# Optimization experiments

Hardware: AMD Instinct MI355X
Metric: run time of the kernel (lower is better)

## Reference

```python
import jax, jax.numpy as jnp
import numpy as np

N = 100000
CIN = 32
COUT = 64
K = 16          # n_kernels (height bins)
STRIDE = 1
DIM = 1         # height coordinate column
XG, ZG, BG = 256, 256, 4   # BEV grid extents and batch size


def setup_inputs() -> dict:
    key = jax.random.key(0)
    k0, k1, k2, k3, k4, k5 = jax.random.split(key, 6)
    feats = jax.random.normal(k0, (N, CIN), dtype=jnp.float32)
    x = jax.random.randint(k1, (N,), 0, XG)
    y = jax.random.randint(k2, (N,), 0, K * STRIDE)
    z = jax.random.randint(k3, (N,), 0, ZG)
    b = jax.random.randint(k4, (N,), 0, BG)
    coords = jnp.stack([x, y, z, b], axis=1).astype(jnp.int32)  # [N,4]
    std = 1.0 / np.sqrt(CIN)
    kernel = jax.random.uniform(k5, (K, CIN, COUT), dtype=jnp.float32,
                                minval=-std, maxval=std)
    return {"feats": feats, "coords": coords, "kernel": kernel}


def reference(feats, coords, kernel):
    # Per-point kernel selection by (quantized) height coordinate.
    idx = coords[:, DIM].astype(jnp.int32) // STRIDE          # [N]
    per_point = kernel[idx]                                   # [N,Cin,Cout] gather
    out = jnp.einsum('ni,nio->no', feats, per_point)          # [N,Cout]
    # Coalesce: zero the height coord and scatter-add duplicate BEV coords.
    # (stride==1 so no spatial re-quantization branch.)
    lin = (coords[:, 3].astype(jnp.int32) * XG + coords[:, 0]) * ZG + coords[:, 2]
    bev = jax.ops.segment_sum(out, lin, num_segments=BG * XG * ZG)  # [B*X*Z,Cout]
    return bev
```

## Files before the change

### kernel.cpp

```cpp
#include <hip/hip_runtime.h>

#define CIN   32
#define COUT  64
#define XG    256
#define ZG    256

__global__ __launch_bounds__(256) void tobev_kernel(
    const float* __restrict__ feats,
    const int*   __restrict__ coords,
    const float* __restrict__ kern,
    float* __restrict__ out,
    int n)
{
    const int wid  = blockIdx.x * 4 + (threadIdx.x >> 6);
    const int lane = threadIdx.x & 63;
    if (wid >= n) return;

    const int4 c = *reinterpret_cast<const int4*>(coords + wid * 4);
    const int idx = c.y;
    const int lin = (c.w * XG + c.x) * ZG + c.z;

    const float f = feats[wid * CIN + (lane & 31)];
    const float* __restrict__ w = kern + idx * (CIN * COUT) + lane;

    float acc = 0.f;
    #pragma unroll
    for (int i = 0; i < CIN; ++i) {
        const float fi = __shfl(f, i, 64);
        acc = fmaf(fi, w[(size_t)i * COUT], acc);
    }

    unsafeAtomicAdd(&out[(size_t)lin * COUT + lane], acc);
}

extern "C" void kernel_launch(void* const* d_in, const int* in_sizes, int n_in,
                              void* d_out, int out_size, void* d_ws, size_t ws_size,
                              hipStream_t stream) {
    const float* feats  = (const float*)d_in[0];
    const int*   coords = (const int*)d_in[1];
    const float* kern   = (const float*)d_in[2];
    float* out = (float*)d_out;

    const int n = in_sizes[0] / CIN;

    hipMemsetAsync(d_out, 0, (size_t)out_size * sizeof(float), stream);

    const int blocks = (n + 3) / 4;
    hipLaunchKernelGGL(tobev_kernel, dim3(blocks), dim3(256), 0, stream,
                       feats, coords, kern, out, n);
}
```

Before: 52.67 us.

## Bucket points by height kernel per wave, keeping weights in registers

Each wave is now assigned one of the K height bins plus a chunk of 256 points. It loads that bin's 32x64 weight slice into registers once, scans the chunk's coords and ballots the points that match, then processes only those. This replaces a per-point gather of the 8KB weight slice with register reuse. The cost is that coords are read K times over, there are K times as many waves, and the serial ballot loop adds control overhead.

```diff
diff --git a/kernel.cpp b/kernel.cpp
--- a/kernel.cpp
+++ b/kernel.cpp
@@ -4,33 +4,51 @@
 #define COUT  64
 #define XG    256
 #define ZG    256
+#define K     16
+#define CHUNK 256
 
-__global__ __launch_bounds__(256) void tobev_kernel(
+__global__ __launch_bounds__(256, 6) void tobev_kernel(
     const float* __restrict__ feats,
     const int*   __restrict__ coords,
     const float* __restrict__ kern,
     float* __restrict__ out,
-    int n)
+    int n, int nchunks)
 {
-    const int wid  = blockIdx.x * 4 + (threadIdx.x >> 6);
+    const int g    = blockIdx.x * 4 + (threadIdx.x >> 6);
     const int lane = threadIdx.x & 63;
-    if (wid >= n) return;
+    const int b    = g / nchunks;
+    const int chunk = g - b * nchunks;
+    if (b >= K) return;
 
-    const int4 c = *reinterpret_cast<const int4*>(coords + wid * 4);
-    const int idx = c.y;
-    const int lin = (c.w * XG + c.x) * ZG + c.z;
+    float w[CIN];
+    #pragma unroll
+    for (int i = 0; i < CIN; ++i)
+        w[i] = kern[(size_t)b * (CIN * COUT) + i * COUT + lane];
 
-    const float f = feats[wid * CIN + (lane & 31)];
-    const float* __restrict__ w = kern + idx * (CIN * COUT) + lane;
+    const int base = chunk * CHUNK;
 
-    float acc = 0.f;
-    #pragma unroll
-    for (int i = 0; i < CIN; ++i) {
-        const float fi = __shfl(f, i, 64);
-        acc = fmaf(fi, w[(size_t)i * COUT], acc);
+    for (int j = 0; j < CHUNK / 64; ++j) {
+        const int p = base + j * 64 + lane;
+        int idx = -1, lin = 0;
+        if (p < n) {
+            const int4 c = *reinterpret_cast<const int4*>(coords + (size_t)p * 4);
+            idx = c.y;
+            lin = (c.w * XG + c.x) * ZG + c.z;
+        }
+        unsigned long long mask = __ballot(idx == b);
+        while (mask) {
+            const int s = __ffsll(mask) - 1;
+            mask &= mask - 1;
+            const int   ps   = base + j * 64 + s;
+            const int   lins = __shfl(lin, s, 64);
+            const float f    = feats[(size_t)ps * CIN + (lane & 31)];
+            float acc = 0.f;
+            #pragma unroll
+            for (int i = 0; i < CIN; ++i)
+                acc = fmaf(__shfl(f, i, 64), w[i], acc);
+            unsafeAtomicAdd(&out[(size_t)lins * COUT + lane], acc);
+        }
     }
-
-    unsafeAtomicAdd(&out[(size_t)lin * COUT + lane], acc);
 }
 
 extern "C" void kernel_launch(void* const* d_in, const int* in_sizes, int n_in,
@@ -45,7 +63,9 @@
 
     hipMemsetAsync(d_out, 0, (size_t)out_size * sizeof(float), stream);
 
-    const int blocks = (n + 3) / 4;
+    const int nchunks = (n + CHUNK - 1) / CHUNK;
+    const int nwaves  = K * nchunks;
+    const int blocks  = (nwaves + 3) / 4;
     hipLaunchKernelGGL(tobev_kernel, dim3(blocks), dim3(256), 0, stream,
-                       feats, coords, kern, out, n);
+                       feats, coords, kern, out, n, nchunks);
 }
```

Result: slower. 76.89 us (+46.0%).

## Bucket points per BEV cell and compute segment sums without output atomics

Applied to the files above, without the earlier changes.

Replaces the per-point atomic scatter with a three-phase scheme. First, points are binned into fixed-capacity slots per BEV cell using counters, with an overflow list for crowded cells. Second, one wave per cell accumulates its points and writes the output directly, with half of the kernel weights staged in LDS. Third, a single block atomically adds the overflow points. This removes the output memset and atomics, but adds a workspace pass, a full-grid sweep over all cells (mostly empty), a single-block serial overflow kernel, and a silent cap on overflow entries.

```diff
diff --git a/kernel.cpp b/kernel.cpp
--- a/kernel.cpp
+++ b/kernel.cpp
@@ -1,11 +1,100 @@
 #include <hip/hip_runtime.h>
 
-#define CIN   32
-#define COUT  64
-#define XG    256
-#define ZG    256
+#define CIN    32
+#define COUT   64
+#define XG     256
+#define ZG     256
+#define K      16
+#define NSEG   (4 * 256 * 256)
+#define MAXPPB 8
+#define MAX_OVF 4096
 
-__global__ __launch_bounds__(256) void tobev_kernel(
+__global__ __launch_bounds__(256) void phaseA(
+    const int* __restrict__ coords,
+    int* __restrict__ counts, int* __restrict__ slots, int* __restrict__ ovf,
+    int n)
+{
+    const int p = blockIdx.x * 256 + threadIdx.x;
+    if (p >= n) return;
+    const int4 c = *reinterpret_cast<const int4*>(coords + (size_t)p * 4);
+    const int lin = (c.w * XG + c.x) * ZG + c.z;
+    const int packed = (c.y << 20) | p;
+    const int pos = atomicAdd(&counts[lin], 1);
+    if (pos < MAXPPB) {
+        slots[(size_t)lin * MAXPPB + pos] = packed;
+    } else {
+        const int o = atomicAdd(&ovf[0], 1);
+        if (o < MAX_OVF) { ovf[64 + 2*o] = lin; ovf[64 + 2*o + 1] = packed; }
+    }
+}
+
+__global__ __launch_bounds__(1024) void phaseB(
+    const float* __restrict__ feats,
+    const float* __restrict__ kern,
+    const int* __restrict__ counts, const int* __restrict__ slots,
+    float* __restrict__ out)
+{
+    __shared__ float wl[8 * CIN * COUT];
+    for (int j = threadIdx.x; j < 8 * CIN * COUT; j += 1024)
+        wl[j] = kern[j];
+    __syncthreads();
+
+    const int wv   = threadIdx.x >> 6;
+    const int lane = threadIdx.x & 63;
+    const int segBase = blockIdx.x * 512 + wv * 32;
+
+    for (int s = 0; s < 32; ++s) {
+        const int seg = segBase + s;
+        int cnt = counts[seg];
+        if (cnt > MAXPPB) cnt = MAXPPB;
+        float acc = 0.f;
+        for (int q = 0; q < cnt; ++q) {
+            const int packed = slots[(size_t)seg * MAXPPB + q];
+            const int pid = packed & 0xFFFFF;
+            const int idx = packed >> 20;
+            const float f = feats[(size_t)pid * CIN + (lane & 31)];
+            if (idx < 8) {
+                const float* __restrict__ w = &wl[idx * (CIN * COUT) + lane];
+                #pragma unroll
+                for (int i = 0; i < CIN; ++i)
+                    acc = fmaf(__shfl(f, i, 64), w[(size_t)i * COUT], acc);
+            } else {
+                const float* __restrict__ w = &kern[(size_t)idx * (CIN * COUT) + lane];
+                #pragma unroll
+                for (int i = 0; i < CIN; ++i)
+                    acc = fmaf(__shfl(f, i, 64), w[(size_t)i * COUT], acc);
+            }
+        }
+        out[(size_t)seg * COUT + lane] = acc;
+    }
+}
+
+__global__ __launch_bounds__(256) void phaseC(
+    const float* __restrict__ feats,
+    const float* __restrict__ kern,
+    const int* __restrict__ ovf,
+    float* __restrict__ out)
+{
+    int nov = ovf[0];
+    if (nov > MAX_OVF) nov = MAX_OVF;
+    const int wv   = threadIdx.x >> 6;
+    const int lane = threadIdx.x & 63;
+    for (int e = wv; e < nov; e += 4) {
+        const int lin    = ovf[64 + 2*e];
+        const int packed = ovf[64 + 2*e + 1];
+        const int pid = packed & 0xFFFFF;
+        const int idx = packed >> 20;
+        const float f = feats[(size_t)pid * CIN + (lane & 31)];
+        const float* __restrict__ w = &kern[(size_t)idx * (CIN * COUT) + lane];
+        float acc = 0.f;
+        #pragma unroll
+        for (int i = 0; i < CIN; ++i)
+            acc = fmaf(__shfl(f, i, 64), w[(size_t)i * COUT], acc);
+        unsafeAtomicAdd(&out[(size_t)lin * COUT + lane], acc);
+    }
+}
+
+__global__ __launch_bounds__(256) void tobev_atomic(
     const float* __restrict__ feats,
     const int*   __restrict__ coords,
     const float* __restrict__ kern,
@@ -15,21 +104,15 @@
     const int wid  = blockIdx.x * 4 + (threadIdx.x >> 6);
     const int lane = threadIdx.x & 63;
     if (wid >= n) return;
-
-    const int4 c = *reinterpret_cast<const int4*>(coords + wid * 4);
+    const int4 c = *reinterpret_cast<const int4*>(coords + (size_t)wid * 4);
     const int idx = c.y;
     const int lin = (c.w * XG + c.x) * ZG + c.z;
-
-    const float f = feats[wid * CIN + (lane & 31)];
-    const float* __restrict__ w = kern + idx * (CIN * COUT) + lane;
-
+    const float f = feats[(size_t)wid * CIN + (lane & 31)];
+    const float* __restrict__ w = kern + (size_t)idx * (CIN * COUT) + lane;
     float acc = 0.f;
     #pragma unroll
-    for (int i = 0; i < CIN; ++i) {
-        const float fi = __shfl(f, i, 64);
-        acc = fmaf(fi, w[(size_t)i * COUT], acc);
-    }
-
+    for (int i = 0; i < CIN; ++i)
+        acc = fmaf(__shfl(f, i, 64), w[(size_t)i * COUT], acc);
     unsafeAtomicAdd(&out[(size_t)lin * COUT + lane], acc);
 }
 
@@ -40,12 +123,26 @@
     const int*   coords = (const int*)d_in[1];
     const float* kern   = (const float*)d_in[2];
     float* out = (float*)d_out;
-
     const int n = in_sizes[0] / CIN;
 
-    hipMemsetAsync(d_out, 0, (size_t)out_size * sizeof(float), stream);
+    const size_t needed = ((size_t)NSEG + 64 + 2 * MAX_OVF + (size_t)NSEG * MAXPPB) * 4;
 
-    const int blocks = (n + 3) / 4;
-    hipLaunchKernelGGL(tobev_kernel, dim3(blocks), dim3(256), 0, stream,
-                       feats, coords, kern, out, n);
+    if (ws_size >= needed) {
+        int* ws     = (int*)d_ws;
+        int* counts = ws;
+        int* ovf    = ws + NSEG;
+        int* slots  = ws + NSEG + 64 + 2 * MAX_OVF;
+
+        hipMemsetAsync(counts, 0, ((size_t)NSEG + 64) * 4, stream);
+        hipLaunchKernelGGL(phaseA, dim3((n + 255) / 256), dim3(256), 0, stream,
+                           coords, counts, slots, ovf, n);
+        hipLaunchKernelGGL(phaseB, dim3(NSEG / 512), dim3(1024), 0, stream,
+                           feats, kern, counts, slots, out);
+        hipLaunchKernelGGL(phaseC, dim3(1), dim3(256), 0, stream,
+                           feats, kern, ovf, out);
+    } else {
+        hipMemsetAsync(d_out, 0, (size_t)out_size * sizeof(float), stream);
+        hipLaunchKernelGGL(tobev_atomic, dim3((n + 3) / 4), dim3(256), 0, stream,
+                           feats, coords, kern, out, n);
+    }
 }
```

Result: slower. 76.25 us (+44.8%).

## Group points by kernel bin per wave to reuse weights in registers

Applied to the files above, without the earlier changes.

Each wavefront now takes 64 points instead of one. It uses ballots to group points that share the same height-bin kernel, loads that bin's weight slice into registers once per group, and then loops over the group's points serially. Each point's features are read with vectorized loads and the partial sums are reduced with cross-lane shuffles before the atomic adds. This cuts redundant weight loads and wave-launch overhead, but it makes the per-point work serial within a wave and launches far fewer waves, so latency may be poorly hidden.

```diff
diff --git a/kernel.cpp b/kernel.cpp
--- a/kernel.cpp
+++ b/kernel.cpp
@@ -5,32 +5,75 @@
 #define XG    256
 #define ZG    256
 
-__global__ __launch_bounds__(256) void tobev_kernel(
+__global__ __launch_bounds__(256) void tobev_dedup(
     const float* __restrict__ feats,
     const int*   __restrict__ coords,
     const float* __restrict__ kern,
     float* __restrict__ out,
     int n)
 {
-    const int wid  = blockIdx.x * 4 + (threadIdx.x >> 6);
+    const int wv   = threadIdx.x >> 6;
     const int lane = threadIdx.x & 63;
-    if (wid >= n) return;
+    const int wid  = blockIdx.x * 4 + wv;
+    const int base = wid * 64;
 
-    const int4 c = *reinterpret_cast<const int4*>(coords + wid * 4);
-    const int idx = c.y;
-    const int lin = (c.w * XG + c.x) * ZG + c.z;
+    int m = n - base;
+    m = m < 0 ? 0 : (m > 64 ? 64 : m);
+    if (m == 0) return;
 
-    const float f = feats[wid * CIN + (lane & 31)];
-    const float* __restrict__ w = kern + idx * (CIN * COUT) + lane;
+    const int g = lane >> 4;
+    const int q = lane & 15;
 
-    float acc = 0.f;
-    #pragma unroll
-    for (int i = 0; i < CIN; ++i) {
-        const float fi = __shfl(f, i, 64);
-        acc = fmaf(fi, w[(size_t)i * COUT], acc);
+    int idx_v = 0, lin_v = 0;
+    if (lane < m) {
+        const int4 c = *reinterpret_cast<const int4*>(coords + (size_t)(base + lane) * 4);
+        idx_v = c.y;
+        lin_v = (c.w * XG + c.x) * ZG + c.z;
     }
 
-    unsafeAtomicAdd(&out[(size_t)lin * COUT + lane], acc);
+    unsigned long long done = (m >= 64) ? 0ull : (~0ull << m);
+
+    while (done != ~0ull) {
+        const int p0   = __ffsll((unsigned long long)~done) - 1;
+        const int bidx = __shfl(idx_v, p0, 64);
+        unsigned long long bm = __ballot(idx_v == bidx) & ~done;
+        done |= bm;
+
+        const float* __restrict__ wb = kern + (size_t)bidx * (CIN * COUT) + 512 * g + 4 * q;
+        float4 wq[8];
+        #pragma unroll
+        for (int j = 0; j < 8; ++j)
+            wq[j] = *reinterpret_cast<const float4*>(wb + 64 * j);
+
+        while (bm) {
+            const int p = __ffsll(bm) - 1;
+            bm &= bm - 1;
+            const int lin = __shfl(lin_v, p, 64);
+            const int ps  = base + p;
+
+            const float* __restrict__ fp = feats + (size_t)ps * CIN + 8 * g;
+            const float4 fA = *reinterpret_cast<const float4*>(fp);
+            const float4 fB = *reinterpret_cast<const float4*>(fp + 4);
+            const float fs[8] = {fA.x, fA.y, fA.z, fA.w, fB.x, fB.y, fB.z, fB.w};
+
+            float a0 = 0.f, a1 = 0.f, a2 = 0.f, a3 = 0.f;
+            #pragma unroll
+            for (int j = 0; j < 8; ++j) {
+                const float fb = fs[j];
+                a0 = fmaf(fb, wq[j].x, a0);
+                a1 = fmaf(fb, wq[j].y, a1);
+                a2 = fmaf(fb, wq[j].z, a2);
+                a3 = fmaf(fb, wq[j].w, a3);
+            }
+            a0 += __shfl_xor(a0, 16, 64); a0 += __shfl_xor(a0, 32, 64);
+            a1 += __shfl_xor(a1, 16, 64); a1 += __shfl_xor(a1, 32, 64);
+            a2 += __shfl_xor(a2, 16, 64); a2 += __shfl_xor(a2, 32, 64);
+            a3 += __shfl_xor(a3, 16, 64); a3 += __shfl_xor(a3, 32, 64);
+
+            const float v = (g == 0) ? a0 : (g == 1) ? a1 : (g == 2) ? a2 : a3;
+            unsafeAtomicAdd(&out[(size_t)lin * COUT + 4 * q + g], v);
+        }
+    }
 }
 
 extern "C" void kernel_launch(void* const* d_in, const int* in_sizes, int n_in,
@@ -40,12 +83,12 @@
     const int*   coords = (const int*)d_in[1];
     const float* kern   = (const float*)d_in[2];
     float* out = (float*)d_out;
-
     const int n = in_sizes[0] / CIN;
 
     hipMemsetAsync(d_out, 0, (size_t)out_size * sizeof(float), stream);
 
-    const int blocks = (n + 3) / 4;
-    hipLaunchKernelGGL(tobev_kernel, dim3(blocks), dim3(256), 0, stream,
+    const int nwaves = (n + 63) / 64;
+    const int blocks = (nwaves + 3) / 4;
+    hipLaunchKernelGGL(tobev_dedup, dim3(blocks), dim3(256), 0, stream,
                        feats, coords, kern, out, n);
 }
```

Result: slower. 58.62 us (+11.3%).
